# Performance work log

Hardware: AMD Instinct MI355X
Metric: run time of the kernel (lower is better)

Reference implementation:

```python
import jax, jax.numpy as jnp
import numpy as np


def log_g(x):
    # log of g(x) = where(x>=0, x+0.5, sigmoid(x))
    return jnp.where(x >= 0, jnp.log(jax.nn.relu(x) + 0.5), -jax.nn.softplus(-x))


def setup_inputs() -> dict:
    key = jax.random.key(0)
    ks = jax.random.split(key, 6)
    B, S, D, Din = 4, 4096, 1024, 2048
    x = jax.random.normal(ks[0], (B, S, D), jnp.float32)
    s1 = 1.0 / np.sqrt(D)
    W1 = jax.random.normal(ks[1], (D, 3 * Din), jnp.float32) * s1
    b1 = jax.random.normal(ks[2], (3 * Din,), jnp.float32) * s1
    b1 = b1.at[Din:2 * Din].add(1.0)  # forget_bias_init_scale = 1.0
    s2 = 1.0 / np.sqrt(Din)
    W2 = jax.random.normal(ks[3], (Din, D), jnp.float32) * s2
    b2 = jax.random.normal(ks[4], (D,), jnp.float32) * s2
    init_h = jax.random.normal(ks[5], (Din,), jnp.float32)
    return {"x": x, "W1": W1, "b1": b1, "W2": W2, "b2": b2, "init_h": init_h}


def reference(x, W1, b1, W2, b2, init_h):
    B, S, _ = x.shape
    Din = init_h.shape[0]
    proj = x @ W1 + b1                              # [B,S,3*Din]
    hidden, forget_gate, input_gate = jnp.split(proj, 3, axis=-1)
    # use_coeff_norm = True branch (normalized gates in log space)
    diff = jax.nn.softplus(-forget_gate) - jax.nn.softplus(-input_gate)
    log_coeffs = -jax.nn.softplus(diff)             # log(f/(f+i))
    log_val_coeffs = -jax.nn.softplus(-diff)        # log(i/(f+i))
    log_values = log_val_coeffs + log_g(hidden)     # [B,S,Din]
    # prepend learned initial hidden state
    prev_log_hidden = jnp.broadcast_to(log_g(init_h), (B, 1, Din))
    log_values = jnp.concatenate([prev_log_hidden, log_values], axis=1)  # [B,S+1,Din]
    log_coeffs = jnp.pad(log_coeffs, ((0, 0), (1, 0), (0, 0)))           # [B,S+1,Din]
    # heinsen associative scan in log space
    a_star = jnp.cumsum(log_coeffs, axis=1)
    log_h = a_star + jax.lax.cumlogsumexp(log_values - a_star, axis=1)
    out_h = jnp.exp(log_h[:, -S:])                  # [B,S,Din]
    next_hidden = out_h[:, -1:]
    next_log_hidden = log_h[:, -1:]
    out = out_h @ W2 + b2                           # [B,S,D]
    return (out, next_hidden, next_log_hidden)
```

## Files before the change

kernel.cpp:

```cpp
#include <hip/hip_runtime.h>
#include <cstdint>
#include <cstddef>

#define BB 4
#define SS 4096
#define DD 1024
#define DIN 2048
#define MTOT (BB*SS)
#define K1 DD
#define K2 DIN
#define N2 DD
#define NCH (BB*DIN)
#define NCHUNK 32
#define CLEN (SS/NCHUNK)

typedef _Float16 half8  __attribute__((ext_vector_type(8)));
typedef _Float16 half4v __attribute__((ext_vector_type(4)));
typedef float    floatx4 __attribute__((ext_vector_type(4)));

#define AS1(p) ((__attribute__((address_space(1))) void*)(uintptr_t)(p))
#define AS3(p) ((__attribute__((address_space(3))) void*)(uint32_t)(uintptr_t)(p))

__device__ __forceinline__ void gload16(const void* g, void* l) {
  __builtin_amdgcn_global_load_lds(AS1(g), AS3(l), 16, 0, 0);
}

__device__ __forceinline__ float sigm(float x) { return 1.f / (1.f + __expf(-x)); }
__device__ __forceinline__ float softp(float x) {
  return fmaxf(x, 0.f) + __logf(1.f + __expf(-fabsf(x)));
}
__device__ __forceinline__ uint32_t hbits(float f) {
  _Float16 h = (_Float16)f; uint16_t u; __builtin_memcpy(&u, &h, 2); return (uint32_t)u;
}
__device__ __forceinline__ float h_lo(uint32_t v) {
  uint16_t u = (uint16_t)(v & 0xffffu); _Float16 h; __builtin_memcpy(&h, &u, 2); return (float)h;
}
__device__ __forceinline__ float h_hi(uint32_t v) {
  uint16_t u = (uint16_t)(v >> 16); _Float16 h; __builtin_memcpy(&h, &u, 2); return (float)h;
}


__global__ void f32_to_f16_vec(const float* __restrict__ src, _Float16* __restrict__ dst) {
  int i = (blockIdx.x * blockDim.x + threadIdx.x) * 4;
  float4 v = *(const float4*)(src + i);
  half4v o; o.x = (_Float16)v.x; o.y = (_Float16)v.y; o.z = (_Float16)v.z; o.w = (_Float16)v.w;
  *(half4v*)(dst + i) = o;
}

__global__ void transpose_cvt(const float* __restrict__ src, _Float16* __restrict__ dst,
                              int R, int C) {
  __shared__ float t[32][33];
  int c0 = blockIdx.x * 32, r0 = blockIdx.y * 32;
  int tx = threadIdx.x, ty = threadIdx.y;
#pragma unroll
  for (int j = 0; j < 32; j += 8)
    t[ty + j][tx] = src[(size_t)(r0 + ty + j) * C + c0 + tx];
  __syncthreads();
#pragma unroll
  for (int j = 0; j < 32; j += 8)
    dst[(size_t)(c0 + ty + j) * R + r0 + tx] = (_Float16)t[tx][ty + j];
}

__global__ __launch_bounds__(256) void gemm1_fused(
    const _Float16* __restrict__ xh, const _Float16* __restrict__ w1t,
    const float* __restrict__ b1, uint32_t* __restrict__ zg) {
  __shared__ _Float16 As[128 * 32];
  __shared__ _Float16 Bs[3][64 * 32];

  const int tid = threadIdx.x;
  const int wave = tid >> 6, lane = tid & 63;
  const int wm = wave >> 1, wn = wave & 1;
  const int m0 = blockIdx.y * 128;
  const int d0 = blockIdx.x * 64;
  const int lrow = lane >> 2;
  const int lk = (lane & 3) * 8;
  const int kq = (lane >> 4) * 8;

  floatx4 acc[3][4][2] = {};

  for (int k0 = 0; k0 < K1; k0 += 32) {
    __syncthreads();
#pragma unroll
    for (int i = 0; i < 2; ++i) {
      int chunk = wave * 2 + i;
      const _Float16* g = xh + (size_t)(m0 + chunk * 16 + lrow) * K1 + k0 + lk;
      gload16(g, As + chunk * 512);
    }
#pragma unroll
    for (int gt = 0; gt < 3; ++gt) {
      const _Float16* g = w1t + (size_t)(gt * DIN + d0 + wave * 16 + lrow) * K1 + k0 + lk;
      gload16(g, &Bs[gt][wave * 512]);
    }
    __syncthreads();

    half8 af[4], bfr[3][2];
#pragma unroll
    for (int mi = 0; mi < 4; ++mi)
      af[mi] = *(const half8*)(As + (wm * 64 + mi * 16 + (lane & 15)) * 32 + kq);
#pragma unroll
    for (int gt = 0; gt < 3; ++gt)
#pragma unroll
      for (int ni = 0; ni < 2; ++ni)
        bfr[gt][ni] = *(const half8*)(&Bs[gt][(wn * 32 + ni * 16 + (lane & 15)) * 32 + kq]);
#pragma unroll
    for (int gt = 0; gt < 3; ++gt)
#pragma unroll
      for (int mi = 0; mi < 4; ++mi)
#pragma unroll
        for (int ni = 0; ni < 2; ++ni)
          acc[gt][mi][ni] = __builtin_amdgcn_mfma_f32_16x16x32_f16(
              af[mi], bfr[gt][ni], acc[gt][mi][ni], 0, 0, 0);
  }

#pragma unroll
  for (int ni = 0; ni < 2; ++ni) {
    int d = d0 + wn * 32 + ni * 16 + (lane & 15);
    float bh = b1[d], bf_ = b1[DIN + d], bi = b1[2 * DIN + d];
#pragma unroll
    for (int mi = 0; mi < 4; ++mi) {
#pragma unroll
      for (int r = 0; r < 4; ++r) {
        int m = m0 + wm * 64 + mi * 16 + (lane >> 4) * 4 + r;
        float hv = acc[0][mi][ni][r] + bh;
        float fv = acc[1][mi][ni][r] + bf_;
        float iv = acc[2][mi][ni][r] + bi;
        float dff = softp(-fv) - softp(-iv);
        float z = sigm(dff);
        float gg = (hv >= 0.f) ? (hv + 0.5f) : sigm(hv);
        zg[(size_t)m * DIN + d] = hbits(z) | (hbits(gg) << 16);
      }
    }
  }
}


__global__ void scanA(const uint32_t* __restrict__ zg,
                      float* __restrict__ cA, float* __restrict__ cB) {
  int gidx = blockIdx.x * 256 + threadIdx.x;
  int q = gidx >> 13, c = gidx & (NCH - 1);
  int b = c >> 11, d = c & (DIN - 1);
  size_t base = ((size_t)b * SS + q * CLEN) * DIN + d;
  float A = 1.f, Bv = 0.f;
#pragma unroll 4
  for (int t = 0; t < CLEN; ++t) {
    uint32_t v = zg[base + (size_t)t * DIN];
    float z = h_lo(v), g = h_hi(v);
    A *= (1.f - z);
    Bv = fmaf(z, g - Bv, Bv);
  }
  cA[q * NCH + c] = A;
  cB[q * NCH + c] = Bv;
}

__global__ void scanB(const float* __restrict__ cA, const float* __restrict__ cB,
                      const float* __restrict__ init_h, float* __restrict__ cH) {
  int c = blockIdx.x * 256 + threadIdx.x;
  int d = c & (DIN - 1);
  float x = init_h[d];
  float h = (x >= 0.f) ? (x + 0.5f) : sigm(x);
#pragma unroll
  for (int q = 0; q < NCHUNK; ++q) {
    cH[q * NCH + c] = h;
    h = fmaf(cA[q * NCH + c], h, cB[q * NCH + c]);
  }
}

__global__ void scanC(const uint32_t* __restrict__ zg, const float* __restrict__ cH,
                      _Float16* __restrict__ hh, float* __restrict__ out_tail) {
  int gidx = blockIdx.x * 256 + threadIdx.x;
  int q = gidx >> 13, c = gidx & (NCH - 1);
  int b = c >> 11, d = c & (DIN - 1);
  size_t base = ((size_t)b * SS + q * CLEN) * DIN + d;
  float h = cH[q * NCH + c];
#pragma unroll 4
  for (int t = 0; t < CLEN; ++t) {
    uint32_t v = zg[base + (size_t)t * DIN];
    float z = h_lo(v), g = h_hi(v);
    h = fmaf(z, g - h, h);
    hh[base + (size_t)t * DIN] = (_Float16)h;
  }
  if (q == NCHUNK - 1) {
    out_tail[c] = h;
    out_tail[NCH + c] = logf(h);
  }
}

__global__ __launch_bounds__(256) void gemm2k(
    const _Float16* __restrict__ hh, const _Float16* __restrict__ w2t,
    const float* __restrict__ b2, float* __restrict__ out) {
  __shared__ _Float16 As[128 * 32];
  __shared__ _Float16 Bs[128 * 32];

  const int tid = threadIdx.x;
  const int wave = tid >> 6, lane = tid & 63;
  const int wm = wave >> 1, wn = wave & 1;
  const int m0 = blockIdx.y * 128;
  const int n0 = blockIdx.x * 128;
  const int lrow = lane >> 2;
  const int lk = (lane & 3) * 8;
  const int kq = (lane >> 4) * 8;

  floatx4 acc[4][4] = {};

  for (int k0 = 0; k0 < K2; k0 += 32) {
    __syncthreads();
#pragma unroll
    for (int i = 0; i < 2; ++i) {
      int chunk = wave * 2 + i;
      const _Float16* gA = hh + (size_t)(m0 + chunk * 16 + lrow) * K2 + k0 + lk;
      gload16(gA, As + chunk * 512);
      const _Float16* gB = w2t + (size_t)(n0 + chunk * 16 + lrow) * K2 + k0 + lk;
      gload16(gB, Bs + chunk * 512);
    }
    __syncthreads();

    half8 af[4], bfr[4];
#pragma unroll
    for (int mi = 0; mi < 4; ++mi)
      af[mi] = *(const half8*)(As + (wm * 64 + mi * 16 + (lane & 15)) * 32 + kq);
#pragma unroll
    for (int ni = 0; ni < 4; ++ni)
      bfr[ni] = *(const half8*)(Bs + (wn * 64 + ni * 16 + (lane & 15)) * 32 + kq);
#pragma unroll
    for (int mi = 0; mi < 4; ++mi)
#pragma unroll
      for (int ni = 0; ni < 4; ++ni)
        acc[mi][ni] = __builtin_amdgcn_mfma_f32_16x16x32_f16(af[mi], bfr[ni], acc[mi][ni], 0, 0, 0);
  }

#pragma unroll
  for (int ni = 0; ni < 4; ++ni) {
    int n = n0 + wn * 64 + ni * 16 + (lane & 15);
    float bias = b2[n];
#pragma unroll
    for (int mi = 0; mi < 4; ++mi) {
#pragma unroll
      for (int r = 0; r < 4; ++r) {
        int m = m0 + wm * 64 + mi * 16 + (lane >> 4) * 4 + r;
        out[(size_t)m * N2 + n] = acc[mi][ni][r] + bias;
      }
    }
  }
}


extern "C" void kernel_launch(void* const* d_in, const int* in_sizes, int n_in,
                              void* d_out, int out_size, void* d_ws, size_t ws_size,
                              hipStream_t stream) {
  const float* x      = (const float*)d_in[0];
  const float* W1     = (const float*)d_in[1];
  const float* b1     = (const float*)d_in[2];
  const float* W2     = (const float*)d_in[3];
  const float* b2     = (const float*)d_in[4];
  const float* init_h = (const float*)d_in[5];
  float* out = (float*)d_out;

  char* w = (char*)d_ws;
  _Float16* xh  = (_Float16*)w; w += (size_t)MTOT * K1 * 2;
  _Float16* w1t = (_Float16*)w; w += (size_t)3 * DIN * K1 * 2;
  _Float16* w2t = (_Float16*)w; w += (size_t)N2 * K2 * 2;
  uint32_t* zg  = (uint32_t*)w; w += (size_t)MTOT * DIN * 4;
  _Float16* hh  = (_Float16*)w; w += (size_t)MTOT * DIN * 2;
  float* cA = (float*)w; w += (size_t)NCH * NCHUNK * 4;
  float* cB = (float*)w; w += (size_t)NCH * NCHUNK * 4;
  float* cH = (float*)w; w += (size_t)NCH * NCHUNK * 4;

  f32_to_f16_vec<<<dim3(MTOT * K1 / 1024), dim3(256), 0, stream>>>(x, xh);
  transpose_cvt<<<dim3(3 * DIN / 32, K1 / 32), dim3(32, 8), 0, stream>>>(W1, w1t, K1, 3 * DIN);
  transpose_cvt<<<dim3(N2 / 32, K2 / 32), dim3(32, 8), 0, stream>>>(W2, w2t, K2, N2);

  gemm1_fused<<<dim3(DIN / 64, MTOT / 128), dim3(256), 0, stream>>>(xh, w1t, b1, zg);

  scanA<<<dim3(NCH * NCHUNK / 256), dim3(256), 0, stream>>>(zg, cA, cB);
  scanB<<<dim3(NCH / 256), dim3(256), 0, stream>>>(cA, cB, init_h, cH);
  scanC<<<dim3(NCH * NCHUNK / 256), dim3(256), 0, stream>>>(zg, cH, hh, out + (size_t)MTOT * DD);

  gemm2k<<<dim3(N2 / 128, MTOT / 128), dim3(256), 0, stream>>>(hh, w2t, b2, out);
}
```

Baseline: 618.6 us.

## Swizzle LDS tiles in both GEMMs, add explicit vmcnt wait, simplify gate math

```diff
diff --git a/kernel.cpp b/kernel.cpp
--- a/kernel.cpp
+++ b/kernel.cpp
@@ -26,9 +26,6 @@
 }
 
 __device__ __forceinline__ float sigm(float x) { return 1.f / (1.f + __expf(-x)); }
-__device__ __forceinline__ float softp(float x) {
-  return fmaxf(x, 0.f) + __logf(1.f + __expf(-fabsf(x)));
-}
 __device__ __forceinline__ uint32_t hbits(float f) {
   _Float16 h = (_Float16)f; uint16_t u; __builtin_memcpy(&u, &h, 2); return (uint32_t)u;
 }
@@ -73,8 +70,8 @@
   const int m0 = blockIdx.y * 128;
   const int d0 = blockIdx.x * 64;
   const int lrow = lane >> 2;
-  const int lk = (lane & 3) * 8;
-  const int kq = (lane >> 4) * 8;
+  const int lk = (((lane & 3) ^ (lrow & 3)) * 8);
+  const int roff = ((((lane & 15) << 2) | ((lane >> 4) ^ (lane & 3))) * 8);
 
   floatx4 acc[3][4][2] = {};
 
@@ -83,25 +80,24 @@
 #pragma unroll
     for (int i = 0; i < 2; ++i) {
       int chunk = wave * 2 + i;
-      const _Float16* g = xh + (size_t)(m0 + chunk * 16 + lrow) * K1 + k0 + lk;
-      gload16(g, As + chunk * 512);
-    }
-#pragma unroll
-    for (int gt = 0; gt < 3; ++gt) {
-      const _Float16* g = w1t + (size_t)(gt * DIN + d0 + wave * 16 + lrow) * K1 + k0 + lk;
-      gload16(g, &Bs[gt][wave * 512]);
-    }
+      gload16(xh + (size_t)(m0 + chunk * 16 + lrow) * K1 + k0 + lk, As + chunk * 512);
+    }
+#pragma unroll
+    for (int gt = 0; gt < 3; ++gt)
+      gload16(w1t + (size_t)(gt * DIN + d0 + wave * 16 + lrow) * K1 + k0 + lk,
+              &Bs[gt][wave * 512]);
+    asm volatile("s_waitcnt vmcnt(0)" ::: "memory");
     __syncthreads();
 
     half8 af[4], bfr[3][2];
 #pragma unroll
     for (int mi = 0; mi < 4; ++mi)
-      af[mi] = *(const half8*)(As + (wm * 64 + mi * 16 + (lane & 15)) * 32 + kq);
+      af[mi] = *(const half8*)(As + (wm * 4 + mi) * 512 + roff);
 #pragma unroll
     for (int gt = 0; gt < 3; ++gt)
 #pragma unroll
       for (int ni = 0; ni < 2; ++ni)
-        bfr[gt][ni] = *(const half8*)(&Bs[gt][(wn * 32 + ni * 16 + (lane & 15)) * 32 + kq]);
+        bfr[gt][ni] = *(const half8*)(&Bs[gt][(wn * 2 + ni) * 512 + roff]);
 #pragma unroll
     for (int gt = 0; gt < 3; ++gt)
 #pragma unroll
@@ -124,9 +120,11 @@
         float hv = acc[0][mi][ni][r] + bh;
         float fv = acc[1][mi][ni][r] + bf_;
         float iv = acc[2][mi][ni][r] + bi;
-        float dff = softp(-fv) - softp(-iv);
-        float z = sigm(dff);
-        float gg = (hv >= 0.f) ? (hv + 0.5f) : sigm(hv);
+        float u = 1.f + __expf(-fminf(fmaxf(fv, -30.f), 30.f));
+        float v = 1.f + __expf(-fminf(fmaxf(iv, -30.f), 30.f));
+        float z = __fdividef(u, u + v);
+        float gg = (hv >= 0.f) ? (hv + 0.5f)
+                               : __fdividef(1.f, 1.f + __expf(-fmaxf(hv, -30.f)));
         zg[(size_t)m * DIN + d] = hbits(z) | (hbits(gg) << 16);
       }
     }
@@ -197,8 +195,8 @@
   const int m0 = blockIdx.y * 128;
   const int n0 = blockIdx.x * 128;
   const int lrow = lane >> 2;
-  const int lk = (lane & 3) * 8;
-  const int kq = (lane >> 4) * 8;
+  const int lk = (((lane & 3) ^ (lrow & 3)) * 8);
+  const int roff = ((((lane & 15) << 2) | ((lane >> 4) ^ (lane & 3))) * 8);
 
   floatx4 acc[4][4] = {};
 
@@ -207,20 +205,19 @@
 #pragma unroll
     for (int i = 0; i < 2; ++i) {
       int chunk = wave * 2 + i;
-      const _Float16* gA = hh + (size_t)(m0 + chunk * 16 + lrow) * K2 + k0 + lk;
-      gload16(gA, As + chunk * 512);
-      const _Float16* gB = w2t + (size_t)(n0 + chunk * 16 + lrow) * K2 + k0 + lk;
-      gload16(gB, Bs + chunk * 512);
-    }
+      gload16(hh  + (size_t)(m0 + chunk * 16 + lrow) * K2 + k0 + lk, As + chunk * 512);
+      gload16(w2t + (size_t)(n0 + chunk * 16 + lrow) * K2 + k0 + lk, Bs + chunk * 512);
+    }
+    asm volatile("s_waitcnt vmcnt(0)" ::: "memory");
     __syncthreads();
 
     half8 af[4], bfr[4];
 #pragma unroll
     for (int mi = 0; mi < 4; ++mi)
-      af[mi] = *(const half8*)(As + (wm * 64 + mi * 16 + (lane & 15)) * 32 + kq);
+      af[mi] = *(const half8*)(As + (wm * 4 + mi) * 512 + roff);
 #pragma unroll
     for (int ni = 0; ni < 4; ++ni)
-      bfr[ni] = *(const half8*)(Bs + (wn * 64 + ni * 16 + (lane & 15)) * 32 + kq);
+      bfr[ni] = *(const half8*)(Bs + (wn * 4 + ni) * 512 + roff);
 #pragma unroll
     for (int mi = 0; mi < 4; ++mi)
 #pragma unroll
```

New measurement: 594.0 us. 4.0% less time.
